# Optimization experiments

Measured on AMD Instinct MI355X. Metric: run time of the kernel, lower is better.

## Reference

```python
import jax, jax.numpy as jnp
import numpy as np

NUM_CLASSES = 1000
ATTR_EMBED_DIM = 128
DIM_Z = 512
DIM_G = 1024
INIT_STD = 0.2
SCALING = 1.0
REGULARIZE_G = 1.0
EPS = 1e-6


def setup_inputs() -> dict:
    key = jax.random.key(0)
    ks = jax.random.split(key, 6)
    B, C, P = 8, 4, 512
    qz = jax.random.normal(ks[0], (B, C, P, DIM_Z), dtype=jnp.float32)
    attr_idx = jax.random.randint(ks[1], (B,), 0, NUM_CLASSES)
    W_base = INIT_STD * jax.random.normal(ks[2], (DIM_G, DIM_Z), dtype=jnp.float32)
    embed_table = jax.random.normal(ks[3], (NUM_CLASSES, ATTR_EMBED_DIM), dtype=jnp.float32)
    lim_u = 1.0 / np.sqrt(ATTR_EMBED_DIM)
    Wu = jax.random.uniform(ks[4], (DIM_G, ATTR_EMBED_DIM), minval=-lim_u, maxval=lim_u, dtype=jnp.float32)
    Wv = jax.random.uniform(ks[5], (DIM_Z, ATTR_EMBED_DIM), minval=-lim_u, maxval=lim_u, dtype=jnp.float32)
    return {"qz": qz, "attr_idx": attr_idx, "W_base": W_base,
            "embed_table": embed_table, "Wu": Wu, "Wv": Wv}


def _abs_norm(x):
    # relu in fp32, then L1-normalize along last dim (torch F.normalize p=1)
    x = jax.nn.relu(x.astype(jnp.float32))
    denom = jnp.maximum(jnp.sum(jnp.abs(x), axis=-1, keepdims=True), EPS)
    return x / denom


def reference(qz, attr_idx, W_base, embed_table, Wu, Wv):
    a_emb = embed_table[attr_idx]                 # [B, E]
    u = a_emb @ Wu.T                              # [B, G]
    v = a_emb @ Wv.T                              # [B, D]
    # Per-sample rank-1 perturbed factor: W = W_base + u \otimes v  -> [B, G, D]
    W = W_base[None, :, :] + u[:, :, None] * v[:, None, :]
    qg = jnp.einsum('bcpd,bgd->bcpg', qz, W) * SCALING
    qg = _abs_norm(qg / REGULARIZE_G)
    return jnp.einsum('bcpg,bgd->bcpd', qg, W) * SCALING
```

## Files before the change

### kernel.cpp

```cpp
#include <hip/hip_runtime.h>
#include <hip/hip_bf16.h>

#define BATCH   8
#define MROWS   2048
#define MTOT    16384
#define DIM_Z   512
#define DIM_G   1024
#define EDIM    128
#define EPS     1e-6f
#define BK      64

typedef unsigned short u16;
typedef unsigned int   u32;
typedef __attribute__((ext_vector_type(8))) short bf16x8;
typedef __attribute__((ext_vector_type(4))) float f32x4;

__device__ __forceinline__ u16 f2b(float f) {
    u32 x = __float_as_uint(f);
    u32 r = x + 0x7fffu + ((x >> 16) & 1u);
    return (u16)(r >> 16);
}

__device__ __forceinline__ u32 cvtpk(float lo, float hi) {
    u32 r;
    asm("v_cvt_pk_bf16_f32 %0, %1, %2" : "=v"(r) : "v"(lo), "v"(hi));
    return r;
}

#define GLD16(gsrc, ldst) __builtin_amdgcn_global_load_lds( \
    (const __attribute__((address_space(1))) unsigned int*)(gsrc), \
    (__attribute__((address_space(3))) unsigned int*)(ldst), 16, 0, 0)

__global__ void uv_kernel(const float* __restrict__ emb, const int* __restrict__ idx,
                          const float* __restrict__ Wu, const float* __restrict__ Wv,
                          float* __restrict__ u, float* __restrict__ v,
                          float* __restrict__ rsum) {
    __shared__ float a[EDIM];
    int b = blockIdx.y;
    int t = threadIdx.x;
    if (blockIdx.x == 0)
        for (int i = t; i < MROWS; i += 256) rsum[(size_t)b * MROWS + i] = 0.f;
    if (t < EDIM) a[t] = emb[(size_t)idx[b] * EDIM + t];
    __syncthreads();
    int tx = t & 31, ty = t >> 5;
    int oBase = blockIdx.x * 256;
    for (int o0 = 0; o0 < 256; o0 += 8) {
        int o = oBase + o0 + ty;
        const float* wrow = (o < DIM_G) ? (Wu + (size_t)o * EDIM)
                                        : (Wv + (size_t)(o - DIM_G) * EDIM);
        float s = 0.f;
#pragma unroll
        for (int q = 0; q < 4; ++q) s += a[q * 32 + tx] * wrow[q * 32 + tx];
        s += __shfl_xor(s, 1, 64);
        s += __shfl_xor(s, 2, 64);
        s += __shfl_xor(s, 4, 64);
        s += __shfl_xor(s, 8, 64);
        s += __shfl_xor(s, 16, 64);
        if (tx == 0) {
            if (o < DIM_G) u[b * DIM_G + o] = s;
            else           v[b * DIM_Z + (o - DIM_G)] = s;
        }
    }
}

__global__ void wpack_kernel(const float* __restrict__ Wbase,
                             const float* __restrict__ u, const float* __restrict__ v,
                             u16* __restrict__ W, u16* __restrict__ WT) {
    __shared__ u16 tile[32][33];
    int h = blockIdx.x;
    int b = h & 7, t8 = h >> 3;
    int d0 = (t8 & 15) * 32, g0 = (t8 >> 4) * 32;
    int tx = threadIdx.x, ty = threadIdx.y;
    float vb = v[b * DIM_Z + d0 + tx];
#pragma unroll
    for (int j = 0; j < 4; ++j) {
        int g = g0 + ty + j * 8;
        u16 h16 = f2b(Wbase[(size_t)g * DIM_Z + d0 + tx] + u[b * DIM_G + g] * vb);
        W[((size_t)b * DIM_G + g) * DIM_Z + d0 + tx] = h16;
        tile[ty + j * 8][tx] = h16;
    }
    __syncthreads();
#pragma unroll
    for (int j = 0; j < 4; ++j)
        WT[((size_t)b * DIM_Z + d0 + ty + j * 8) * DIM_G + g0 + tx] =
            tile[tx][ty + j * 8];
}

__global__ __launch_bounds__(256, 2)
void gemm1(const float* __restrict__ qz, const u16* __restrict__ Wall,
           u16* __restrict__ qg, float* __restrict__ rsum) {
    const int N = DIM_G, K = DIM_Z;
    __shared__ u16 As[128 * BK];
    __shared__ u16 Bs[256 * BK];

    int h = blockIdx.x;
    int xcd = h & 7, idx = h >> 3;
    int tile = xcd * 64 + idx;
    int mBase = (tile >> 2) * 128;
    int nBase = (tile & 3) * 256;
    int b = mBase >> 11;

    int tid  = threadIdx.x;
    int lane = tid & 63, wid = tid >> 6;
    int wm = wid >> 1, wn = wid & 1;
    int lr = lane & 15, lg = lane >> 4;

    f32x4 acc[4][8] = {};

    int sRow = tid >> 3;
    int sC   = tid & 7;
    int cw   = sC ^ (sRow & 7);
    const float* aSrc = qz + (size_t)(mBase + sRow) * K + sC * 8;
    const u16*   bSrc = Wall + (size_t)b * DIM_G * DIM_Z
                             + (size_t)(nBase + sRow) * K + cw * 8;

    for (int kt = 0; kt < K; kt += BK) {
        float4 alo[4], ahi[4];
#pragma unroll
        for (int r = 0; r < 4; ++r) {
            const float* g = aSrc + (size_t)r * 32 * K + kt;
            alo[r] = *(const float4*)g;
            ahi[r] = *(const float4*)(g + 4);
        }
        __syncthreads();
#pragma unroll
        for (int r = 0; r < 8; ++r)
            GLD16(bSrc + (size_t)r * 32 * K + kt, &Bs[(r * 256 + wid * 64) * 8]);
#pragma unroll
        for (int r = 0; r < 4; ++r) {
            uint4 q;
            q.x = cvtpk(alo[r].x, alo[r].y);
            q.y = cvtpk(alo[r].z, alo[r].w);
            q.z = cvtpk(ahi[r].x, ahi[r].y);
            q.w = cvtpk(ahi[r].z, ahi[r].w);
            *(uint4*)&As[(r * 32 + sRow) * BK + cw * 8] = q;
        }
        __syncthreads();
#pragma unroll
        for (int ks = 0; ks < 2; ++ks) {
            bf16x8 af[4], bfr[8];
#pragma unroll
            for (int mi = 0; mi < 4; ++mi) {
                int row = wm * 64 + mi * 16 + lr;
                int cq  = (ks * 4 + lg) ^ (row & 7);
                af[mi] = *(const bf16x8*)&As[row * BK + cq * 8];
            }
#pragma unroll
            for (int ni = 0; ni < 8; ++ni) {
                int row = wn * 128 + ni * 16 + lr;
                int cq  = (ks * 4 + lg) ^ (row & 7);
                bfr[ni] = *(const bf16x8*)&Bs[row * BK + cq * 8];
            }
            __builtin_amdgcn_s_setprio(1);
#pragma unroll
            for (int mi = 0; mi < 4; ++mi)
#pragma unroll
                for (int ni = 0; ni < 8; ++ni)
                    acc[mi][ni] = __builtin_amdgcn_mfma_f32_16x16x32_bf16(
                        af[mi], bfr[ni], acc[mi][ni], 0, 0, 0);
            __builtin_amdgcn_s_setprio(0);
        }
    }

    int mw = mBase + wm * 64, nw = nBase + wn * 128;
#pragma unroll
    for (int mi = 0; mi < 4; ++mi)
#pragma unroll
        for (int r = 0; r < 4; ++r) {
            int m = mw + mi * 16 + lg * 4 + r;
            float vals[8];
            float s = 0.f;
#pragma unroll
            for (int ni = 0; ni < 8; ++ni) {
                vals[ni] = fmaxf(acc[mi][ni][r], 0.f);
                s += vals[ni];
            }
#pragma unroll
            for (int ni = 0; ni < 8; ++ni)
                qg[(size_t)m * N + nw + ni * 16 + lr] = f2b(vals[ni]);
            s += __shfl_xor(s, 1, 64);
            s += __shfl_xor(s, 2, 64);
            s += __shfl_xor(s, 4, 64);
            s += __shfl_xor(s, 8, 64);
            if (lr == 0) atomicAdd(&rsum[m], s);
        }
}

__global__ __launch_bounds__(256, 4)
void gemm2(const u16* __restrict__ qg, const u16* __restrict__ WTall,
           const float* __restrict__ rsum, float* __restrict__ out) {
    const int N = DIM_Z, K = DIM_G;
    __shared__ u16 As[128 * BK];
    __shared__ u16 Bs[128 * BK];

    int h = blockIdx.x;
    int xcd = h & 7, idx = h >> 3;
    int tile = xcd * 64 + idx;
    int mBase = (tile >> 2) * 128;
    int nBase = (tile & 3) * 128;
    int b = mBase >> 11;

    int tid  = threadIdx.x;
    int lane = tid & 63, wid = tid >> 6;
    int wm = wid >> 1, wn = wid & 1;
    int lr = lane & 15, lg = lane >> 4;

    f32x4 acc[4][4] = {};

    int sRow = tid >> 3;
    int cw   = (tid & 7) ^ (sRow & 7);
    const u16* aSrc = qg + (size_t)(mBase + sRow) * K + cw * 8;
    const u16* bSrc = WTall + (size_t)b * DIM_Z * DIM_G
                            + (size_t)(nBase + sRow) * K + cw * 8;

    for (int kt = 0; kt < K; kt += BK) {
        __syncthreads();
#pragma unroll
        for (int r = 0; r < 4; ++r) {
            GLD16(aSrc + (size_t)r * 32 * K + kt, &As[(r * 256 + wid * 64) * 8]);
            GLD16(bSrc + (size_t)r * 32 * K + kt, &Bs[(r * 256 + wid * 64) * 8]);
        }
        __syncthreads();
#pragma unroll
        for (int ks = 0; ks < 2; ++ks) {
            bf16x8 af[4], bfr[4];
#pragma unroll
            for (int mi = 0; mi < 4; ++mi) {
                int row = wm * 64 + mi * 16 + lr;
                int cq  = (ks * 4 + lg) ^ (row & 7);
                af[mi] = *(const bf16x8*)&As[row * BK + cq * 8];
            }
#pragma unroll
            for (int ni = 0; ni < 4; ++ni) {
                int row = wn * 64 + ni * 16 + lr;
                int cq  = (ks * 4 + lg) ^ (row & 7);
                bfr[ni] = *(const bf16x8*)&Bs[row * BK + cq * 8];
            }
            __builtin_amdgcn_s_setprio(1);
#pragma unroll
            for (int mi = 0; mi < 4; ++mi)
#pragma unroll
                for (int ni = 0; ni < 4; ++ni)
                    acc[mi][ni] = __builtin_amdgcn_mfma_f32_16x16x32_bf16(
                        af[mi], bfr[ni], acc[mi][ni], 0, 0, 0);
            __builtin_amdgcn_s_setprio(0);
        }
    }

    int mw = mBase + wm * 64, nw = nBase + wn * 64;
#pragma unroll
    for (int mi = 0; mi < 4; ++mi)
#pragma unroll
        for (int r = 0; r < 4; ++r) {
            int m = mw + mi * 16 + lg * 4 + r;
            float inv = 1.f / fmaxf(rsum[m], EPS);
#pragma unroll
            for (int ni = 0; ni < 4; ++ni)
                __builtin_nontemporal_store(acc[mi][ni][r] * inv,
                    &out[(size_t)m * N + nw + ni * 16 + lr]);
        }
}

extern "C" void kernel_launch(void* const* d_in, const int* in_sizes, int n_in,
                              void* d_out, int out_size, void* d_ws, size_t ws_size,
                              hipStream_t stream) {
    const float* qz    = (const float*)d_in[0];
    const int*   attr  = (const int*)d_in[1];
    const float* Wbase = (const float*)d_in[2];
    const float* emb   = (const float*)d_in[3];
    const float* Wu    = (const float*)d_in[4];
    const float* Wv    = (const float*)d_in[5];
    float* out = (float*)d_out;

    char* ws = (char*)d_ws;
    size_t off = 0;
    auto alloc = [&](size_t bytes) -> void* {
        void* p = ws + off;
        off = (off + bytes + 255) & ~(size_t)255;
        return p;
    };
    float* u    = (float*)alloc((size_t)BATCH * DIM_G * 4);
    float* v    = (float*)alloc((size_t)BATCH * DIM_Z * 4);
    float* rsum = (float*)alloc((size_t)MTOT * 4);
    u16*   W    = (u16*)  alloc((size_t)BATCH * DIM_G * DIM_Z * 2);
    u16*   WT   = (u16*)  alloc((size_t)BATCH * DIM_G * DIM_Z * 2);
    u16*   qg   = (u16*)  alloc((size_t)MTOT * DIM_G * 2);
    if (off > ws_size) return;

    uv_kernel<<<dim3(6, BATCH), dim3(256), 0, stream>>>(emb, attr, Wu, Wv, u, v, rsum);

    wpack_kernel<<<dim3(4096), dim3(32, 8), 0, stream>>>(Wbase, u, v, W, WT);

    gemm1<<<dim3(512), dim3(256), 0, stream>>>(qz, W, qg, rsum);

    gemm2<<<dim3(512), dim3(256), 0, stream>>>(qg, WT, rsum, out);
}
```

Baseline: 81.32 us.

## Fuse both GEMMs into one persistent kernel with per-row-tile completion counters

Merges gemm1 and gemm2 into a single launch. Each block computes its slice of qg, signals an atomic counter for its 128-row tile, and spin-waits until all four N-slices of that tile are done before running the second GEMM on the same rows. This removes one kernel launch and the grid-wide barrier between the GEMMs, and keeps qg for that tile hot in L2. The spin-wait assumes all four cooperating blocks are co-resident, which risks deadlock if the grid is not fully resident. Phase 2 now runs under the gemm1 launch bounds rather than gemm2's higher occupancy.

```diff
diff --git a/kernel.cpp b/kernel.cpp
--- a/kernel.cpp
+++ b/kernel.cpp
@@ -34,12 +34,14 @@
 __global__ void uv_kernel(const float* __restrict__ emb, const int* __restrict__ idx,
                           const float* __restrict__ Wu, const float* __restrict__ Wv,
                           float* __restrict__ u, float* __restrict__ v,
-                          float* __restrict__ rsum) {
+                          float* __restrict__ rsum, u32* __restrict__ done) {
     __shared__ float a[EDIM];
     int b = blockIdx.y;
     int t = threadIdx.x;
-    if (blockIdx.x == 0)
+    if (blockIdx.x == 0) {
         for (int i = t; i < MROWS; i += 256) rsum[(size_t)b * MROWS + i] = 0.f;
+        if (t < 16) done[b * 16 + t] = 0;
+    }
     if (t < EDIM) a[t] = emb[(size_t)idx[b] * EDIM + t];
     __syncthreads();
     int tx = t & 31, ty = t >> 5;
@@ -87,178 +89,176 @@
 }
 
 __global__ __launch_bounds__(256, 2)
-void gemm1(const float* __restrict__ qz, const u16* __restrict__ Wall,
-           u16* __restrict__ qg, float* __restrict__ rsum) {
-    const int N = DIM_G, K = DIM_Z;
+void gemm_fused(const float* __restrict__ qz, const u16* __restrict__ Wall,
+                const u16* __restrict__ WTall, u16* __restrict__ qg,
+                float* __restrict__ rsum, float* __restrict__ out,
+                u32* __restrict__ done) {
     __shared__ u16 As[128 * BK];
     __shared__ u16 Bs[256 * BK];
 
     int h = blockIdx.x;
-    int xcd = h & 7, idx = h >> 3;
-    int tile = xcd * 64 + idx;
-    int mBase = (tile >> 2) * 128;
-    int nBase = (tile & 3) * 256;
-    int b = mBase >> 11;
+    int xcd = h & 7, j = h >> 3;
+    int mT = j >> 2, q = j & 3;
+    int b = xcd;
+    int mBase = (xcd * 16 + mT) * 128;
 
     int tid  = threadIdx.x;
     int lane = tid & 63, wid = tid >> 6;
     int wm = wid >> 1, wn = wid & 1;
     int lr = lane & 15, lg = lane >> 4;
 
-    f32x4 acc[4][8] = {};
-
     int sRow = tid >> 3;
     int sC   = tid & 7;
     int cw   = sC ^ (sRow & 7);
-    const float* aSrc = qz + (size_t)(mBase + sRow) * K + sC * 8;
-    const u16*   bSrc = Wall + (size_t)b * DIM_G * DIM_Z
-                             + (size_t)(nBase + sRow) * K + cw * 8;
-
-    for (int kt = 0; kt < K; kt += BK) {
-        float4 alo[4], ahi[4];
-#pragma unroll
-        for (int r = 0; r < 4; ++r) {
-            const float* g = aSrc + (size_t)r * 32 * K + kt;
-            alo[r] = *(const float4*)g;
-            ahi[r] = *(const float4*)(g + 4);
+
+    {
+        const int N = DIM_G, K = DIM_Z;
+        int nBase = q * 256;
+        f32x4 acc[4][8] = {};
+        const float* aSrc = qz + (size_t)(mBase + sRow) * K + sC * 8;
+        const u16*   bSrc = Wall + (size_t)b * DIM_G * DIM_Z
+                                 + (size_t)(nBase + sRow) * K + cw * 8;
+
+        for (int kt = 0; kt < K; kt += BK) {
+            float4 alo[4], ahi[4];
+#pragma unroll
+            for (int r = 0; r < 4; ++r) {
+                const float* g = aSrc + (size_t)r * 32 * K + kt;
+                alo[r] = *(const float4*)g;
+                ahi[r] = *(const float4*)(g + 4);
+            }
+            __syncthreads();
+#pragma unroll
+            for (int r = 0; r < 8; ++r)
+                GLD16(bSrc + (size_t)r * 32 * K + kt, &Bs[(r * 256 + wid * 64) * 8]);
+#pragma unroll
+            for (int r = 0; r < 4; ++r) {
+                uint4 qv;
+                qv.x = cvtpk(alo[r].x, alo[r].y);
+                qv.y = cvtpk(alo[r].z, alo[r].w);
+                qv.z = cvtpk(ahi[r].x, ahi[r].y);
+                qv.w = cvtpk(ahi[r].z, ahi[r].w);
+                *(uint4*)&As[(r * 32 + sRow) * BK + cw * 8] = qv;
+            }
+            __syncthreads();
+#pragma unroll
+            for (int ks = 0; ks < 2; ++ks) {
+                bf16x8 af[4], bfr[8];
+#pragma unroll
+                for (int mi = 0; mi < 4; ++mi) {
+                    int row = wm * 64 + mi * 16 + lr;
+                    int cq  = (ks * 4 + lg) ^ (row & 7);
+                    af[mi] = *(const bf16x8*)&As[row * BK + cq * 8];
+                }
+#pragma unroll
+                for (int ni = 0; ni < 8; ++ni) {
+                    int row = wn * 128 + ni * 16 + lr;
+                    int cq  = (ks * 4 + lg) ^ (row & 7);
+                    bfr[ni] = *(const bf16x8*)&Bs[row * BK + cq * 8];
+                }
+                __builtin_amdgcn_s_setprio(1);
+#pragma unroll
+                for (int mi = 0; mi < 4; ++mi)
+#pragma unroll
+                    for (int ni = 0; ni < 8; ++ni)
+                        acc[mi][ni] = __builtin_amdgcn_mfma_f32_16x16x32_bf16(
+                            af[mi], bfr[ni], acc[mi][ni], 0, 0, 0);
+                __builtin_amdgcn_s_setprio(0);
+            }
         }
-        __syncthreads();
-#pragma unroll
-        for (int r = 0; r < 8; ++r)
-            GLD16(bSrc + (size_t)r * 32 * K + kt, &Bs[(r * 256 + wid * 64) * 8]);
-#pragma unroll
-        for (int r = 0; r < 4; ++r) {
-            uint4 q;
-            q.x = cvtpk(alo[r].x, alo[r].y);
-            q.y = cvtpk(alo[r].z, alo[r].w);
-            q.z = cvtpk(ahi[r].x, ahi[r].y);
-            q.w = cvtpk(ahi[r].z, ahi[r].w);
-            *(uint4*)&As[(r * 32 + sRow) * BK + cw * 8] = q;
+
+        int mw = mBase + wm * 64, nw = q * 256 + wn * 128;
+#pragma unroll
+        for (int mi = 0; mi < 4; ++mi)
+#pragma unroll
+            for (int r = 0; r < 4; ++r) {
+                int m = mw + mi * 16 + lg * 4 + r;
+                float vals[8];
+                float s = 0.f;
+#pragma unroll
+                for (int ni = 0; ni < 8; ++ni) {
+                    vals[ni] = fmaxf(acc[mi][ni][r], 0.f);
+                    s += vals[ni];
+                }
+#pragma unroll
+                for (int ni = 0; ni < 8; ++ni)
+                    qg[(size_t)m * N + nw + ni * 16 + lr] = f2b(vals[ni]);
+                s += __shfl_xor(s, 1, 64);
+                s += __shfl_xor(s, 2, 64);
+                s += __shfl_xor(s, 4, 64);
+                s += __shfl_xor(s, 8, 64);
+                if (lr == 0) atomicAdd(&rsum[m], s);
+            }
+    }
+
+    __threadfence();
+    __syncthreads();
+    if (tid == 0)
+        __hip_atomic_fetch_add(&done[xcd * 16 + mT], 1u,
+                               __ATOMIC_RELEASE, __HIP_MEMORY_SCOPE_AGENT);
+
+    if (tid == 0) {
+        while (__hip_atomic_load(&done[xcd * 16 + mT],
+                                 __ATOMIC_ACQUIRE, __HIP_MEMORY_SCOPE_AGENT) < 4u)
+            __builtin_amdgcn_s_sleep(8);
+    }
+    __syncthreads();
+
+    {
+        const int N = DIM_Z, K = DIM_G;
+        int nBase = q * 128;
+        f32x4 acc[4][4] = {};
+        const u16* aSrc = qg + (size_t)(mBase + sRow) * K + cw * 8;
+        const u16* bSrc = WTall + (size_t)b * DIM_Z * DIM_G
+                                + (size_t)(nBase + sRow) * K + cw * 8;
+
+        for (int kt = 0; kt < K; kt += BK) {
+            __syncthreads();
+#pragma unroll
+            for (int r = 0; r < 4; ++r) {
+                GLD16(aSrc + (size_t)r * 32 * K + kt, &As[(r * 256 + wid * 64) * 8]);
+                GLD16(bSrc + (size_t)r * 32 * K + kt, &Bs[(r * 256 + wid * 64) * 8]);
+            }
+            __syncthreads();
+#pragma unroll
+            for (int ks = 0; ks < 2; ++ks) {
+                bf16x8 af[4], bfr[4];
+#pragma unroll
+                for (int mi = 0; mi < 4; ++mi) {
+                    int row = wm * 64 + mi * 16 + lr;
+                    int cq  = (ks * 4 + lg) ^ (row & 7);
+                    af[mi] = *(const bf16x8*)&As[row * BK + cq * 8];
+                }
+#pragma unroll
+                for (int ni = 0; ni < 4; ++ni) {
+                    int row = wn * 64 + ni * 16 + lr;
+                    int cq  = (ks * 4 + lg) ^ (row & 7);
+                    bfr[ni] = *(const bf16x8*)&Bs[row * BK + cq * 8];
+                }
+                __builtin_amdgcn_s_setprio(1);
+#pragma unroll
+                for (int mi = 0; mi < 4; ++mi)
+#pragma unroll
+                    for (int ni = 0; ni < 4; ++ni)
+                        acc[mi][ni] = __builtin_amdgcn_mfma_f32_16x16x32_bf16(
+                            af[mi], bfr[ni], acc[mi][ni], 0, 0, 0);
+                __builtin_amdgcn_s_setprio(0);
+            }
         }
-        __syncthreads();
-#pragma unroll
-        for (int ks = 0; ks < 2; ++ks) {
-            bf16x8 af[4], bfr[8];
-#pragma unroll
-            for (int mi = 0; mi < 4; ++mi) {
-                int row = wm * 64 + mi * 16 + lr;
-                int cq  = (ks * 4 + lg) ^ (row & 7);
-                af[mi] = *(const bf16x8*)&As[row * BK + cq * 8];
-            }
-#pragma unroll
-            for (int ni = 0; ni < 8; ++ni) {
-                int row = wn * 128 + ni * 16 + lr;
-                int cq  = (ks * 4 + lg) ^ (row & 7);
-                bfr[ni] = *(const bf16x8*)&Bs[row * BK + cq * 8];
-            }
-            __builtin_amdgcn_s_setprio(1);
-#pragma unroll
-            for (int mi = 0; mi < 4; ++mi)
-#pragma unroll
-                for (int ni = 0; ni < 8; ++ni)
-                    acc[mi][ni] = __builtin_amdgcn_mfma_f32_16x16x32_bf16(
-                        af[mi], bfr[ni], acc[mi][ni], 0, 0, 0);
-            __builtin_amdgcn_s_setprio(0);
-        }
-    }
-
-    int mw = mBase + wm * 64, nw = nBase + wn * 128;
-#pragma unroll
-    for (int mi = 0; mi < 4; ++mi)
-#pragma unroll
-        for (int r = 0; r < 4; ++r) {
-            int m = mw + mi * 16 + lg * 4 + r;
-            float vals[8];
-            float s = 0.f;
-#pragma unroll
-            for (int ni = 0; ni < 8; ++ni) {
-                vals[ni] = fmaxf(acc[mi][ni][r], 0.f);
-                s += vals[ni];
-            }
-#pragma unroll
-            for (int ni = 0; ni < 8; ++ni)
-                qg[(size_t)m * N + nw + ni * 16 + lr] = f2b(vals[ni]);
-            s += __shfl_xor(s, 1, 64);
-            s += __shfl_xor(s, 2, 64);
-            s += __shfl_xor(s, 4, 64);
-            s += __shfl_xor(s, 8, 64);
-            if (lr == 0) atomicAdd(&rsum[m], s);
-        }
-}
-
-__global__ __launch_bounds__(256, 4)
-void gemm2(const u16* __restrict__ qg, const u16* __restrict__ WTall,
-           const float* __restrict__ rsum, float* __restrict__ out) {
-    const int N = DIM_Z, K = DIM_G;
-    __shared__ u16 As[128 * BK];
-    __shared__ u16 Bs[128 * BK];
-
-    int h = blockIdx.x;
-    int xcd = h & 7, idx = h >> 3;
-    int tile = xcd * 64 + idx;
-    int mBase = (tile >> 2) * 128;
-    int nBase = (tile & 3) * 128;
-    int b = mBase >> 11;
-
-    int tid  = threadIdx.x;
-    int lane = tid & 63, wid = tid >> 6;
-    int wm = wid >> 1, wn = wid & 1;
-    int lr = lane & 15, lg = lane >> 4;
-
-    f32x4 acc[4][4] = {};
-
-    int sRow = tid >> 3;
-    int cw   = (tid & 7) ^ (sRow & 7);
-    const u16* aSrc = qg + (size_t)(mBase + sRow) * K + cw * 8;
-    const u16* bSrc = WTall + (size_t)b * DIM_Z * DIM_G
-                            + (size_t)(nBase + sRow) * K + cw * 8;
-
-    for (int kt = 0; kt < K; kt += BK) {
-        __syncthreads();
-#pragma unroll
-        for (int r = 0; r < 4; ++r) {
-            GLD16(aSrc + (size_t)r * 32 * K + kt, &As[(r * 256 + wid * 64) * 8]);
-            GLD16(bSrc + (size_t)r * 32 * K + kt, &Bs[(r * 256 + wid * 64) * 8]);
-        }
-        __syncthreads();
-#pragma unroll
-        for (int ks = 0; ks < 2; ++ks) {
-            bf16x8 af[4], bfr[4];
-#pragma unroll
-            for (int mi = 0; mi < 4; ++mi) {
-                int row = wm * 64 + mi * 16 + lr;
-                int cq  = (ks * 4 + lg) ^ (row & 7);
-                af[mi] = *(const bf16x8*)&As[row * BK + cq * 8];
-            }
-#pragma unroll
-            for (int ni = 0; ni < 4; ++ni) {
-                int row = wn * 64 + ni * 16 + lr;
-                int cq  = (ks * 4 + lg) ^ (row & 7);
-                bfr[ni] = *(const bf16x8*)&Bs[row * BK + cq * 8];
-            }
-            __builtin_amdgcn_s_setprio(1);
-#pragma unroll
-            for (int mi = 0; mi < 4; ++mi)
+
+        int mw = mBase + wm * 64, nw = nBase + wn * 64;
+#pragma unroll
+        for (int mi = 0; mi < 4; ++mi)
+#pragma unroll
+            for (int r = 0; r < 4; ++r) {
+                int m = mw + mi * 16 + lg * 4 + r;
+                float inv = 1.f / fmaxf(rsum[m], EPS);
 #pragma unroll
                 for (int ni = 0; ni < 4; ++ni)
-                    acc[mi][ni] = __builtin_amdgcn_mfma_f32_16x16x32_bf16(
-                        af[mi], bfr[ni], acc[mi][ni], 0, 0, 0);
-            __builtin_amdgcn_s_setprio(0);
-        }
-    }
-
-    int mw = mBase + wm * 64, nw = nBase + wn * 64;
-#pragma unroll
-    for (int mi = 0; mi < 4; ++mi)
-#pragma unroll
-        for (int r = 0; r < 4; ++r) {
-            int m = mw + mi * 16 + lg * 4 + r;
-            float inv = 1.f / fmaxf(rsum[m], EPS);
-#pragma unroll
-            for (int ni = 0; ni < 4; ++ni)
-                __builtin_nontemporal_store(acc[mi][ni][r] * inv,
-                    &out[(size_t)m * N + nw + ni * 16 + lr]);
-        }
+                    __builtin_nontemporal_store(acc[mi][ni][r] * inv,
+                        &out[(size_t)m * N + nw + ni * 16 + lr]);
+            }
+    }
 }
 
 extern "C" void kernel_launch(void* const* d_in, const int* in_sizes, int n_in,
@@ -282,16 +282,17 @@
     float* u    = (float*)alloc((size_t)BATCH * DIM_G * 4);
     float* v    = (float*)alloc((size_t)BATCH * DIM_Z * 4);
     float* rsum = (float*)alloc((size_t)MTOT * 4);
+    u32*   done = (u32*)  alloc(128 * 4);
     u16*   W    = (u16*)  alloc((size_t)BATCH * DIM_G * DIM_Z * 2);
     u16*   WT   = (u16*)  alloc((size_t)BATCH * DIM_G * DIM_Z * 2);
     u16*   qg   = (u16*)  alloc((size_t)MTOT * DIM_G * 2);
     if (off > ws_size) return;
 
-    uv_kernel<<<dim3(6, BATCH), dim3(256), 0, stream>>>(emb, attr, Wu, Wv, u, v, rsum);
+    uv_kernel<<<dim3(6, BATCH), dim3(256), 0, stream>>>(
+        emb, attr, Wu, Wv, u, v, rsum, done);
 
     wpack_kernel<<<dim3(4096), dim3(32, 8), 0, stream>>>(Wbase, u, v, W, WT);
 
-    gemm1<<<dim3(512), dim3(256), 0, stream>>>(qz, W, qg, rsum);
-
-    gemm2<<<dim3(512), dim3(256), 0, stream>>>(qg, WT, rsum, out);
-}
+    gemm_fused<<<dim3(512), dim3(256), 0, stream>>>(
+        qz, W, WT, qg, rsum, out, done);
+}
```

Result: slower. 169.3 us (+108.1%).
